# Optimization experiments

Hardware: AMD Instinct MI355X
Metric: run time of the kernel (lower is better)

The kernel has to match this reference:

```python
import jax, jax.numpy as jnp
import numpy as np

D_MODEL = 2048
NHEADS = 16
HEAD_DIM = D_MODEL // NHEADS


def setup_inputs() -> dict:
    key = jax.random.key(0)
    kx, kq, kk, kv, ko = jax.random.split(key, 5)
    B, S = 2, 2048
    scale = 1.0 / np.sqrt(D_MODEL)
    return {
        "x": jax.random.normal(kx, (B, S, D_MODEL), dtype=jnp.float32),
        "Wq": jax.random.normal(kq, (D_MODEL, D_MODEL), dtype=jnp.float32) * scale,
        "Wk": jax.random.normal(kk, (D_MODEL, D_MODEL), dtype=jnp.float32) * scale,
        "Wv": jax.random.normal(kv, (D_MODEL, D_MODEL), dtype=jnp.float32) * scale,
        "Wo": jax.random.normal(ko, (D_MODEL, D_MODEL), dtype=jnp.float32) * scale,
    }


def reference(x, Wq, Wk, Wv, Wo):
    B, S, _ = x.shape
    # nn.Linear(bias=False): y = x @ W.T
    q = (x @ Wq.T).reshape(B, S, NHEADS, HEAD_DIM)
    k = (x @ Wk.T).reshape(B, S, NHEADS, HEAD_DIM)
    v = (x @ Wv.T).reshape(B, S, NHEADS, HEAD_DIM)
    sm_scale = 1.0 / np.sqrt(HEAD_DIM)
    # scores: [B, H, S, S]
    scores = jnp.einsum("bqhd,bkhd->bhqk", q, k) * sm_scale
    causal_mask = jnp.tril(jnp.ones((S, S), dtype=bool))  # [S, S]
    scores = jnp.where(causal_mask, scores, jnp.finfo(scores.dtype).min)
    probs = jax.nn.softmax(scores, axis=-1)
    attn = jnp.einsum("bhqk,bkhd->bqhd", probs, v)  # [B, S, H, D]
    out = attn.reshape(B, S, D_MODEL) @ Wo.T
    return out
```

## Files before the change

kernel.cpp:

```cpp
#include <hip/hip_runtime.h>
#include <hip/hip_bf16.h>
#include <type_traits>

#define DEV __device__ __forceinline__

typedef __bf16 bf16x8 __attribute__((ext_vector_type(8)));
typedef float f32x4 __attribute__((ext_vector_type(4)));
typedef float f32x16 __attribute__((ext_vector_type(16)));
typedef unsigned short u16;
typedef unsigned int u32;

DEV u16 f32_to_bf16(float f) {
  union { float f; u32 u; } x; x.f = f;
  u32 r = (x.u + 0x7FFFu + ((x.u >> 16) & 1u)) >> 16;
  return (u16)r;
}

DEV u32 pack2(float a, float b) {
  union { __hip_bfloat162 h; u32 u; } c;
  c.h = __float22bfloat162_rn(float2{a, b});
  return c.u;
}

DEV void ld_lds16(const void* g, void* l) {
  __builtin_amdgcn_global_load_lds(
      (const __attribute__((address_space(1))) u32*)g,
      (__attribute__((address_space(3))) u32*)l, 16, 0, 0);
}

#define MFMA16(a, b, c) __builtin_amdgcn_mfma_f32_16x16x32_bf16(a, b, c, 0, 0, 0)
#define MFMA32(a, b, c) __builtin_amdgcn_mfma_f32_32x32x16_bf16(a, b, c, 0, 0, 0)

__global__ __launch_bounds__(256) void cast_all(
    const float* __restrict__ x,  const float* __restrict__ wq,
    const float* __restrict__ wk, const float* __restrict__ wv,
    const float* __restrict__ wo,
    u16* __restrict__ xb,  u16* __restrict__ wqb, u16* __restrict__ wkb,
    u16* __restrict__ wvb, u16* __restrict__ wob) {
  int bid = blockIdx.x;
  const float* src; u16* dst; int base;
  if (bid < 8192)       { src = x;  dst = xb;  base = bid; }
  else if (bid < 12288) { src = wq; dst = wqb; base = bid - 8192; }
  else if (bid < 16384) { src = wk; dst = wkb; base = bid - 12288; }
  else if (bid < 20480) { src = wv; dst = wvb; base = bid - 16384; }
  else                  { src = wo; dst = wob; base = bid - 20480; }
  int i = (base * 256 + threadIdx.x) * 4;
  float4 v = *reinterpret_cast<const float4*>(src + i);
  ushort4 o;
  o.x = f32_to_bf16(v.x); o.y = f32_to_bf16(v.y);
  o.z = f32_to_bf16(v.z); o.w = f32_to_bf16(v.w);
  *reinterpret_cast<ushort4*>(dst + i) = o;
}

template <typename OutT>
__global__ __launch_bounds__(256) void gemm_nt(const u16* __restrict__ A,
                                               const u16* __restrict__ B,
                                               OutT* __restrict__ C,
                                               OutT* __restrict__ C2,
                                               int M, int N, int K, int ldc,
                                               float oscLo, float oscHi, int nsplit) {
  __shared__ __align__(16) u16 sA[128 * 64];
  __shared__ __align__(16) u16 sB[128 * 64];
  const int tid = threadIdx.x;
  const int lane = tid & 63, wid = tid >> 6;
  const int lo = lane & 15, hi = lane >> 4;
  const int wm = wid >> 1, wn = wid & 1;
  const int m0 = blockIdx.y * 128, n0 = blockIdx.x * 128;

  f32x4 acc[4][4] = {};

  for (int k0 = 0; k0 < K; k0 += 64) {
    __syncthreads();
#pragma unroll
    for (int i = 0; i < 4; ++i) {
      int e16 = i * 256 + tid;
      int r = e16 >> 3;
      int bcol = ((e16 & 7) * 16) ^ ((r & 7) << 4);
      int col = bcol >> 1;
      ld_lds16(A + (size_t)(m0 + r) * K + k0 + col, sA + e16 * 8);
      ld_lds16(B + (size_t)(n0 + r) * K + k0 + col, sB + e16 * 8);
    }
    __syncthreads();
#pragma unroll
    for (int kc = 0; kc < 2; ++kc) {
      bf16x8 a[4], b[4];
#pragma unroll
      for (int i = 0; i < 4; ++i) {
        int row = wm * 64 + i * 16 + lo;
        int boff = ((kc * 32 + hi * 8) * 2) ^ ((row & 7) << 4);
        a[i] = *(const bf16x8*)((const char*)sA + row * 128 + boff);
      }
#pragma unroll
      for (int i = 0; i < 4; ++i) {
        int row = wn * 64 + i * 16 + lo;
        int boff = ((kc * 32 + hi * 8) * 2) ^ ((row & 7) << 4);
        b[i] = *(const bf16x8*)((const char*)sB + row * 128 + boff);
      }
#pragma unroll
      for (int mi = 0; mi < 4; ++mi)
#pragma unroll
        for (int ni = 0; ni < 4; ++ni)
          acc[mi][ni] = MFMA16(a[mi], b[ni], acc[mi][ni]);
    }
  }
#pragma unroll
  for (int ni = 0; ni < 4; ++ni) {
    int colb = n0 + wn * 64 + ni * 16;
    bool lo_side = (colb < nsplit);
    OutT* dst = lo_side ? C : C2;
    float osc = lo_side ? oscLo : oscHi;
    int col = (lo_side ? colb : colb - nsplit) + lo;
#pragma unroll
    for (int mi = 0; mi < 4; ++mi)
#pragma unroll
      for (int r = 0; r < 4; ++r) {
        size_t row = m0 + wm * 64 + mi * 16 + hi * 4 + r;
        float v = acc[mi][ni][r] * osc;
        if constexpr (std::is_same<OutT, float>::value)
          dst[row * ldc + col] = v;
        else
          dst[row * ldc + col] = f32_to_bf16(v);
      }
  }
}

constexpr float RTHR2 = 11.5416f;

__global__ __launch_bounds__(256, 2) void attn_fwd(const u16* __restrict__ Q,
                                                   const u16* __restrict__ K,
                                                   const u16* __restrict__ VT,
                                                   u16* __restrict__ O) {
  __shared__ __align__(16) u16 sK[2][64 * 128];
  __shared__ __align__(16) u16 sV[2][128 * 64];

  const int x = blockIdx.x, h = blockIdx.y, b = blockIdx.z;
  const int qt = b ? x : (15 - x);
  const int tid = threadIdx.x;
  const int lane = tid & 63, wid = tid >> 6;
  const int l31 = lane & 31, hi5 = lane >> 5;

  const size_t baseQK = ((size_t)b * 2048) * 2048 + (size_t)h * 128;
  const size_t baseV  = ((size_t)h * 128) * 4096 + (size_t)b * 2048;
  const int q0 = qt * 128;
  const int qw = q0 + wid * 32;
  const int qg = qw + l31;
  const int nt = 2 * qt + 2;

  bf16x8 qf[8];
#pragma unroll
  for (int kc = 0; kc < 8; ++kc)
    qf[kc] = *(const bf16x8*)(Q + baseQK + (size_t)qg * 2048 + kc * 16 + hi5 * 8);

  f32x16 o[4] = {};
  float m = -INFINITY, ls = 0.f;

  auto stage = [&](int buf, int t) {
    const int kv = t * 64;
#pragma unroll
    for (int i = 0; i < 4; ++i) {
      int e = i * 256 + tid;
      int r = e >> 4;
      int bc = ((e & 15) * 16) ^ ((r & 15) << 4);
      ld_lds16(K + baseQK + (size_t)(kv + r) * 2048 + (bc >> 1), &sK[buf][e * 8]);
    }
#pragma unroll
    for (int i = 0; i < 4; ++i) {
      int e = i * 256 + tid;
      int r = e >> 3;
      int bc = ((e & 7) * 16) ^ ((r & 7) << 4);
      ld_lds16(VT + baseV + (size_t)r * 4096 + kv + (bc >> 1), &sV[buf][e * 8]);
    }
  };

  stage(0, 0);

  for (int t = 0; t < nt; ++t) {
    __syncthreads();
    if (t + 1 < nt) stage((t + 1) & 1, t + 1);
    const int kv0 = t * 64;
    if (kv0 > qw + 31) continue;
    const u16* bK = sK[t & 1];
    const u16* bV = sV[t & 1];

    f32x16 s[2] = {};
    __builtin_amdgcn_s_setprio(1);
#pragma unroll
    for (int kb = 0; kb < 2; ++kb) {
      int row = kb * 32 + l31;
      int rsw = (row & 15) << 4;
#pragma unroll
      for (int kc = 0; kc < 8; ++kc) {
        int bo = (kc * 32 + hi5 * 16) ^ rsw;
        bf16x8 kf = *(const bf16x8*)((const char*)bK + row * 256 + bo);
        s[kb] = MFMA32(kf, qf[kc], s[kb]);
      }
    }
    __builtin_amdgcn_s_setprio(0);

    if (kv0 + 63 > qw) {
#pragma unroll
      for (int kb = 0; kb < 2; ++kb)
#pragma unroll
        for (int j = 0; j < 16; ++j) {
          int keyg = kv0 + kb * 32 + (j & 3) + 8 * (j >> 2) + 4 * hi5;
          s[kb][j] = (keyg > qg) ? -3e38f : s[kb][j];
        }
    }

    float pmax = -3e38f;
#pragma unroll
    for (int kb = 0; kb < 2; ++kb)
#pragma unroll
      for (int j = 0; j < 16; ++j) pmax = fmaxf(pmax, s[kb][j]);
    pmax = fmaxf(pmax, __shfl_xor(pmax, 32));

    if (!__all(pmax - m <= RTHR2)) {
      float mn = fmaxf(m, pmax);
      float fr = exp2f(m - mn);
      ls *= fr;
#pragma unroll
      for (int d = 0; d < 4; ++d) o[d] *= fr;
      m = mn;
    }

    float rs = 0.f;
#pragma unroll
    for (int kb = 0; kb < 2; ++kb)
#pragma unroll
      for (int j = 0; j < 16; ++j) {
        float pv = exp2f(s[kb][j] - m);
        s[kb][j] = pv;
        rs += pv;
      }
    rs += __shfl_xor(rs, 32);
    ls += rs;

    union PF { u32 w[4]; bf16x8 v; };
    PF pf[4];
#pragma unroll
    for (int kb = 0; kb < 2; ++kb)
#pragma unroll
      for (int gp = 0; gp < 2; ++gp) {
        u32 keep[2], send[2];
#pragma unroll
        for (int w = 0; w < 2; ++w) {
          int ja = 8 * gp + 2 * w;
          int jb = 8 * gp + 4 + 2 * w;
          u32 aa = pack2(s[kb][ja], s[kb][ja + 1]);
          u32 bb = pack2(s[kb][jb], s[kb][jb + 1]);
          keep[w] = hi5 ? bb : aa;
          send[w] = hi5 ? aa : bb;
        }
        u32 recv0 = (u32)__shfl_xor((int)send[0], 32);
        u32 recv1 = (u32)__shfl_xor((int)send[1], 32);
        PF& f = pf[2 * kb + gp];
        f.w[0] = hi5 ? recv0 : keep[0];
        f.w[1] = hi5 ? recv1 : keep[1];
        f.w[2] = hi5 ? keep[0] : recv0;
        f.w[3] = hi5 ? keep[1] : recv1;
      }

    __builtin_amdgcn_s_setprio(1);
#pragma unroll
    for (int d = 0; d < 4; ++d) {
      int row = d * 32 + l31;
      int rsw = (row & 7) << 4;
#pragma unroll
      for (int ks = 0; ks < 4; ++ks) {
        int bo = (ks * 32 + hi5 * 16) ^ rsw;
        bf16x8 vf = *(const bf16x8*)((const char*)bV + row * 128 + bo);
        o[d] = MFMA32(vf, pf[ks].v, o[d]);
      }
    }
    __builtin_amdgcn_s_setprio(0);
  }

  float inv = 1.f / ls;
  size_t orow = (size_t)b * 2048 + qg;
#pragma unroll
  for (int d = 0; d < 4; ++d)
#pragma unroll
    for (int G = 0; G < 4; ++G) {
      union { u32 u[2]; ushort4 s4; } st;
      st.u[0] = pack2(o[d][4 * G + 0] * inv, o[d][4 * G + 1] * inv);
      st.u[1] = pack2(o[d][4 * G + 2] * inv, o[d][4 * G + 3] * inv);
      int col = h * 128 + d * 32 + 8 * G + 4 * hi5;
      *(ushort4*)(O + orow * 2048 + col) = st.s4;
    }
}

extern "C" void kernel_launch(void* const* d_in, const int* in_sizes, int n_in,
                              void* d_out, int out_size, void* d_ws, size_t ws_size,
                              hipStream_t stream) {
  const float* x  = (const float*)d_in[0];
  const float* Wq = (const float*)d_in[1];
  const float* Wk = (const float*)d_in[2];
  const float* Wv = (const float*)d_in[3];
  const float* Wo = (const float*)d_in[4];
  float* out = (float*)d_out;

  constexpr int B = 2, S = 2048, D = 2048;
  constexpr int M = B * S;
  constexpr float QSC = 0.12751742f;
  constexpr int NOSPLIT = 1 << 30;

  char* ws = (char*)d_ws;
  u16* xb  = (u16*)ws; ws += (size_t)M * D * 2;
  u16* wqb = (u16*)ws; ws += (size_t)D * D * 2;
  u16* wkb = (u16*)ws; ws += (size_t)D * D * 2;
  u16* wvb = (u16*)ws; ws += (size_t)D * D * 2;
  u16* wob = (u16*)ws; ws += (size_t)D * D * 2;
  u16* q   = (u16*)ws; ws += (size_t)M * D * 2;
  u16* k   = (u16*)ws; ws += (size_t)M * D * 2;
  u16* vT  = (u16*)ws; ws += (size_t)M * D * 2;
  u16* att = (u16*)ws; ws += (size_t)M * D * 2;

  cast_all<<<24576, 256, 0, stream>>>(x, Wq, Wk, Wv, Wo, xb, wqb, wkb, wvb, wob);

  gemm_nt<u16><<<dim3(32, 32), 256, 0, stream>>>(xb, wqb, q, k, M, 2 * D, D, D,
                                                 QSC, 1.0f, D);
  gemm_nt<u16><<<dim3(32, 16), 256, 0, stream>>>(wvb, xb, vT, vT, D, M, D, M,
                                                 1.0f, 1.0f, NOSPLIT);

  attn_fwd<<<dim3(16, 16, B), 256, 0, stream>>>(q, k, vT, att);

  gemm_nt<float><<<dim3(16, 32), 256, 0, stream>>>(att, wob, out, out, M, D, D, D,
                                                   1.0f, 1.0f, NOSPLIT);
}
```

Before: 272.3 us.

## Split QK projection into dedicated kernel, simplify GEMM epilogue, drop setprio

Adds a dedicated gemm_qk kernel that picks the Q or K weight block and output from blockIdx.y, replacing the split-output logic inside the generic GEMM. The generic GEMM epilogue loses its per-column destination/scale selection and loops rows outermost. The attention kernel's K-tile LDS swizzle changes from a 16-row to an 8-row XOR pattern, and the s_setprio calls around the MFMA sections are removed. Together these aim to cut epilogue branching and change LDS bank behaviour and wave scheduling, at the risk of more bank conflicts or lost prioritisation.

```diff
diff --git a/kernel.cpp b/kernel.cpp
--- a/kernel.cpp
+++ b/kernel.cpp
@@ -56,9 +56,7 @@
 __global__ __launch_bounds__(256) void gemm_nt(const u16* __restrict__ A,
                                                const u16* __restrict__ B,
                                                OutT* __restrict__ C,
-                                               OutT* __restrict__ C2,
-                                               int M, int N, int K, int ldc,
-                                               float oscLo, float oscHi, int nsplit) {
+                                               int M, int N, int K, float osc) {
   __shared__ __align__(16) u16 sA[128 * 64];
   __shared__ __align__(16) u16 sB[128 * 64];
   const int tid = threadIdx.x;
@@ -104,24 +102,88 @@
     }
   }
 #pragma unroll
-  for (int ni = 0; ni < 4; ++ni) {
-    int colb = n0 + wn * 64 + ni * 16;
-    bool lo_side = (colb < nsplit);
-    OutT* dst = lo_side ? C : C2;
-    float osc = lo_side ? oscLo : oscHi;
-    int col = (lo_side ? colb : colb - nsplit) + lo;
-#pragma unroll
-    for (int mi = 0; mi < 4; ++mi)
-#pragma unroll
-      for (int r = 0; r < 4; ++r) {
-        size_t row = m0 + wm * 64 + mi * 16 + hi * 4 + r;
+  for (int mi = 0; mi < 4; ++mi)
+#pragma unroll
+    for (int r = 0; r < 4; ++r) {
+      size_t row = m0 + wm * 64 + mi * 16 + hi * 4 + r;
+#pragma unroll
+      for (int ni = 0; ni < 4; ++ni) {
+        int col = n0 + wn * 64 + ni * 16 + lo;
         float v = acc[mi][ni][r] * osc;
         if constexpr (std::is_same<OutT, float>::value)
-          dst[row * ldc + col] = v;
+          C[row * N + col] = v;
         else
-          dst[row * ldc + col] = f32_to_bf16(v);
-      }
+          C[row * N + col] = f32_to_bf16(v);
+      }
+    }
+}
+
+__global__ __launch_bounds__(256) void gemm_qk(const u16* __restrict__ A,
+                                               const u16* __restrict__ Bqk,
+                                               u16* __restrict__ Cq,
+                                               u16* __restrict__ Ck,
+                                               float qsc) {
+  __shared__ __align__(16) u16 sA[128 * 64];
+  __shared__ __align__(16) u16 sB[128 * 64];
+  constexpr int K = 2048, N = 2048;
+  const int tid = threadIdx.x;
+  const int lane = tid & 63, wid = tid >> 6;
+  const int lo = lane & 15, hi = lane >> 4;
+  const int wm = wid >> 1, wn = wid & 1;
+  const int sel = blockIdx.y >> 5;
+  const int m0 = (blockIdx.y & 31) * 128;
+  const int n0 = blockIdx.x * 128;
+  const u16* B = Bqk + (size_t)sel * N * K;
+  u16* C = sel ? Ck : Cq;
+  const float osc = sel ? 1.0f : qsc;
+
+  f32x4 acc[4][4] = {};
+
+  for (int k0 = 0; k0 < K; k0 += 64) {
+    __syncthreads();
+#pragma unroll
+    for (int i = 0; i < 4; ++i) {
+      int e16 = i * 256 + tid;
+      int r = e16 >> 3;
+      int bcol = ((e16 & 7) * 16) ^ ((r & 7) << 4);
+      int col = bcol >> 1;
+      ld_lds16(A + (size_t)(m0 + r) * K + k0 + col, sA + e16 * 8);
+      ld_lds16(B + (size_t)(n0 + r) * K + k0 + col, sB + e16 * 8);
+    }
+    __syncthreads();
+#pragma unroll
+    for (int kc = 0; kc < 2; ++kc) {
+      bf16x8 a[4], b[4];
+#pragma unroll
+      for (int i = 0; i < 4; ++i) {
+        int row = wm * 64 + i * 16 + lo;
+        int boff = ((kc * 32 + hi * 8) * 2) ^ ((row & 7) << 4);
+        a[i] = *(const bf16x8*)((const char*)sA + row * 128 + boff);
+      }
+#pragma unroll
+      for (int i = 0; i < 4; ++i) {
+        int row = wn * 64 + i * 16 + lo;
+        int boff = ((kc * 32 + hi * 8) * 2) ^ ((row & 7) << 4);
+        b[i] = *(const bf16x8*)((const char*)sB + row * 128 + boff);
+      }
+#pragma unroll
+      for (int mi = 0; mi < 4; ++mi)
+#pragma unroll
+        for (int ni = 0; ni < 4; ++ni)
+          acc[mi][ni] = MFMA16(a[mi], b[ni], acc[mi][ni]);
+    }
   }
+#pragma unroll
+  for (int mi = 0; mi < 4; ++mi)
+#pragma unroll
+    for (int r = 0; r < 4; ++r) {
+      size_t row = m0 + wm * 64 + mi * 16 + hi * 4 + r;
+#pragma unroll
+      for (int ni = 0; ni < 4; ++ni) {
+        int col = n0 + wn * 64 + ni * 16 + lo;
+        C[row * N + col] = f32_to_bf16(acc[mi][ni][r] * osc);
+      }
+    }
 }
 
 constexpr float RTHR2 = 11.5416f;
@@ -160,7 +222,7 @@
     for (int i = 0; i < 4; ++i) {
       int e = i * 256 + tid;
       int r = e >> 4;
-      int bc = ((e & 15) * 16) ^ ((r & 15) << 4);
+      int bc = ((e & 15) * 16) ^ ((r & 7) << 4);
       ld_lds16(K + baseQK + (size_t)(kv + r) * 2048 + (bc >> 1), &sK[buf][e * 8]);
     }
 #pragma unroll
@@ -183,11 +245,10 @@
     const u16* bV = sV[t & 1];
 
     f32x16 s[2] = {};
-    __builtin_amdgcn_s_setprio(1);
 #pragma unroll
     for (int kb = 0; kb < 2; ++kb) {
       int row = kb * 32 + l31;
-      int rsw = (row & 15) << 4;
+      int rsw = (row & 7) << 4;
 #pragma unroll
       for (int kc = 0; kc < 8; ++kc) {
         int bo = (kc * 32 + hi5 * 16) ^ rsw;
@@ -195,7 +256,6 @@
         s[kb] = MFMA32(kf, qf[kc], s[kb]);
       }
     }
-    __builtin_amdgcn_s_setprio(0);
 
     if (kv0 + 63 > qw) {
 #pragma unroll
@@ -260,7 +320,6 @@
         f.w[3] = hi5 ? keep[1] : recv1;
       }
 
-    __builtin_amdgcn_s_setprio(1);
 #pragma unroll
     for (int d = 0; d < 4; ++d) {
       int row = d * 32 + l31;
@@ -272,7 +331,6 @@
         o[d] = MFMA32(vf, pf[ks].v, o[d]);
       }
     }
-    __builtin_amdgcn_s_setprio(0);
   }
 
   float inv = 1.f / ls;
@@ -302,7 +360,6 @@
   constexpr int B = 2, S = 2048, D = 2048;
   constexpr int M = B * S;
   constexpr float QSC = 0.12751742f;
-  constexpr int NOSPLIT = 1 << 30;
 
   char* ws = (char*)d_ws;
   u16* xb  = (u16*)ws; ws += (size_t)M * D * 2;
@@ -317,13 +374,10 @@
 
   cast_all<<<24576, 256, 0, stream>>>(x, Wq, Wk, Wv, Wo, xb, wqb, wkb, wvb, wob);
 
-  gemm_nt<u16><<<dim3(32, 32), 256, 0, stream>>>(xb, wqb, q, k, M, 2 * D, D, D,
-                                                 QSC, 1.0f, D);
-  gemm_nt<u16><<<dim3(32, 16), 256, 0, stream>>>(wvb, xb, vT, vT, D, M, D, M,
-                                                 1.0f, 1.0f, NOSPLIT);
+  gemm_qk<<<dim3(16, 64), 256, 0, stream>>>(xb, wqb, q, k, QSC);
+  gemm_nt<u16><<<dim3(32, 16), 256, 0, stream>>>(wvb, xb, vT, D, M, D, 1.0f);
 
   attn_fwd<<<dim3(16, 16, B), 256, 0, stream>>>(q, k, vT, att);
 
-  gemm_nt<float><<<dim3(16, 32), 256, 0, stream>>>(att, wob, out, out, M, D, D, D,
-                                                   1.0f, 1.0f, NOSPLIT);
-}
+  gemm_nt<float><<<dim3(16, 32), 256, 0, stream>>>(att, wob, out, M, D, D, 1.0f);
+}
```

After: 270.8 us. About the same (-0.6%).
